# Kernel optimization log

Measured on AMD Instinct MI355X. Metric: run time of the kernel, lower is better.

The kernel has to match this reference:

```python
import jax, jax.numpy as jnp
import numpy as np

EPS = 1e-12  # F.normalize default eps


def _l2_normalize(x):
    # F.normalize(x, p=2) normalizes over dim=1 (channels) by default
    n = jnp.sqrt(jnp.sum(x * x, axis=1, keepdims=True))
    return x / jnp.maximum(n, EPS)


def _cost_volume(left, right, num_disp):
    # left, right: (N, C, H, W)
    l = _l2_normalize(left)
    r = _l2_normalize(right)
    # dot[n,h,x,y] = sum_c l[n,c,h,x] * r[n,c,h,y]   -> (N, H, W, W)
    dot = jnp.einsum('nchx,nchy->nhxy', l, r)
    W = left.shape[-1]
    x = jnp.arange(W)                                   # (W,)
    j = jnp.arange(num_disp)                            # (D,)
    # torch.diagonal(offset=-j) + F.pad((j,0)) picks dot[..., x, x-j] with zeros for x<j
    idx = jnp.clip(x[None, :] - j[:, None], 0, W - 1)   # (D, W)
    g = dot[:, :, x[None, :], idx]                      # (N, H, D, W)
    valid = (x[None, :] >= j[:, None])                  # (D, W)
    g = jnp.where(valid[None, None, :, :], g, jnp.zeros((), dtype=g.dtype))
    return jnp.transpose(g, (0, 2, 1, 3))               # (N, D, H, W)


def setup_inputs() -> dict:
    key = jax.random.key(0)
    ks = jax.random.split(key, 6)
    shapes = [(2, 32, 256, 512), (2, 64, 128, 256), (2, 96, 64, 128)]
    inp = {}
    for i, s in enumerate(shapes):
        inp[f'left{i}'] = jax.random.normal(ks[2 * i], s, dtype=jnp.float32)
        inp[f'right{i}'] = jax.random.normal(ks[2 * i + 1], s, dtype=jnp.float32)
    inp['max_disparity'] = 128
    return inp


def reference(left0, right0, left1, right1, left2, right2, max_disparity):
    lefts = [left0, left1, left2]
    rights = [right0, right1, right2]
    md = min(int(max_disparity), lefts[0].shape[-1])
    cost_volumes = []
    for i, (l, r) in enumerate(zip(lefts, rights)):
        cost_volumes.append(_cost_volume(l, r, md // (2 ** i)))
    return tuple(cost_volumes)
```

## Files before the change

kernel.cpp:

```cpp
#include <hip/hip_runtime.h>

typedef __attribute__((ext_vector_type(8))) short bf16x8;
typedef __attribute__((ext_vector_type(4))) float f32x4;

static __device__ __forceinline__ unsigned short f32_to_bf16(float f) {
    unsigned int x = __float_as_uint(f);
    x += 0x7fffu + ((x >> 16) & 1u);
    return (unsigned short)(x >> 16);
}

template<int C, int H, int W, int D, int TX, int NT>
__global__ __launch_bounds__(NT)
void cost_volume_mfma(const float* __restrict__ Lp, const float* __restrict__ Rp,
                      float* __restrict__ out)
{
    constexpr int RS = TX + D;
    constexpr int AS = C + 8;
    constexpr int KC = C / 32;
    constexpr int NW = NT / 64;
    static_assert(NW == TX / 16, "one wave per 16-wide x-tile");
    static_assert((AS * 2) % 16 == 0, "frag rows must be 16B aligned");

    constexpr int STAGE_F = C * (TX + RS);
    constexpr int OBUF_F  = D * TX;
    constexpr int UNION_F = STAGE_F > OBUF_F ? STAGE_F : OBUF_F;

    __shared__ __align__(16) float uni[UNION_F];
    __shared__ __align__(16) unsigned short Abf[RS * AS];
    __shared__ __align__(16) unsigned short Bbf[TX * AS];

    float* lsf  = uni;
    float* rsf  = uni + C * TX;
    float* obuf = uni;

    const int tid = threadIdx.x;
    constexpr int NXB = W / TX;
    const int bx = blockIdx.x;
    const int xb = bx % NXB;
    const int h  = (bx / NXB) % H;
    const int n  = bx / (NXB * H);
    const int X0 = xb * TX;

    for (int i = tid; i < C * TX / 4; i += NT) {
        const int c = i / (TX / 4), v = i % (TX / 4);
        *(float4*)&lsf[c * TX + 4 * v] =
            *(const float4*)&Lp[(((size_t)n * C + c) * H + h) * W + X0 + 4 * v];
    }
    for (int i = tid; i < C * RS / 4; i += NT) {
        const int c = i / (RS / 4), v = i % (RS / 4);
        const int y = X0 - D + 4 * v;
        const float* src = &Rp[(((size_t)n * C + c) * H + h) * W];
        float4 val;
        if (y >= 0) val = *(const float4*)&src[y];
        else {
            val.x = (y + 0) >= 0 ? src[y + 0] : 0.f;
            val.y = (y + 1) >= 0 ? src[y + 1] : 0.f;
            val.z = (y + 2) >= 0 ? src[y + 2] : 0.f;
            val.w = (y + 3) >= 0 ? src[y + 3] : 0.f;
        }
        *(float4*)&rsf[c * RS + 4 * v] = val;
    }
    __syncthreads();

    for (int col = tid; col < TX + RS; col += NT) {
        const float* src; int stride; unsigned short* dst;
        if (col < TX) { src = lsf + col;        stride = TX; dst = Bbf + col * AS; }
        else          { src = rsf + (col - TX); stride = RS; dst = Abf + (col - TX) * AS; }
        float v[C];
        float s = 0.f;
        #pragma unroll
        for (int c = 0; c < C; ++c) { v[c] = src[c * stride]; s += v[c] * v[c]; }
        const float inv = 1.0f / fmaxf(sqrtf(s), 1e-12f);
        #pragma unroll
        for (int c0 = 0; c0 < C; c0 += 8) {
            union { unsigned short us[8]; uint4 q; } p;
            #pragma unroll
            for (int k = 0; k < 8; ++k) p.us[k] = f32_to_bf16(v[c0 + k] * inv);
            *(uint4*)&dst[c0] = p.q;
        }
    }
    __syncthreads();

    const int wave = tid >> 6, lane = tid & 63;
    const int colc = lane & 15, quad = lane >> 4;

    bf16x8 bfr[KC];
    #pragma unroll
    for (int kc = 0; kc < KC; ++kc)
        bfr[kc] = *(const bf16x8*)&Bbf[(wave * 16 + colc) * AS + kc * 32 + quad * 8];

    const int xl = wave * 16 + colc;
    #pragma unroll
    for (int t = 0; t <= D / 16; ++t) {
        const int yt = wave + t;
        f32x4 acc = {0.f, 0.f, 0.f, 0.f};
        #pragma unroll
        for (int kc = 0; kc < KC; ++kc) {
            const bf16x8 a =
                *(const bf16x8*)&Abf[(yt * 16 + colc) * AS + kc * 32 + quad * 8];
            acc = __builtin_amdgcn_mfma_f32_16x16x32_bf16(a, bfr[kc], acc, 0, 0, 0);
        }
        const int jb = D + xl - yt * 16 - quad * 4;
        #pragma unroll
        for (int r = 0; r < 4; ++r) {
            const int j = jb - r;
            if (j >= 0 && j < D) obuf[j * TX + xl] = acc[r];
        }
    }
    __syncthreads();

    constexpr int JV = TX / 4;
    for (int i = tid; i < D * TX / 4; i += NT) {
        const int j = i / JV, c4 = i % JV;
        *(float4*)&out[(((size_t)n * D + j) * H + h) * W + X0 + 4 * c4] =
            *(const float4*)&obuf[j * TX + 4 * c4];
    }
}

extern "C" void kernel_launch(void* const* d_in, const int* in_sizes, int n_in,
                              void* d_out, int out_size, void* d_ws, size_t ws_size,
                              hipStream_t stream) {
    (void)in_sizes; (void)n_in; (void)d_ws; (void)ws_size; (void)out_size;
    const float* l0 = (const float*)d_in[0];
    const float* r0 = (const float*)d_in[1];
    const float* l1 = (const float*)d_in[2];
    const float* r1 = (const float*)d_in[3];
    const float* l2 = (const float*)d_in[4];
    const float* r2 = (const float*)d_in[5];

    float* o0 = (float*)d_out;
    float* o1 = o0 + (size_t)2 * 128 * 256 * 512;
    float* o2 = o1 + (size_t)2 * 64 * 128 * 256;

    cost_volume_mfma<32, 256, 512, 128, 64, 256>
        <<<2 * 256 * (512 / 64), 256, 0, stream>>>(l0, r0, o0);
    cost_volume_mfma<64, 128, 256, 64, 32, 128>
        <<<2 * 128 * (256 / 32), 128, 0, stream>>>(l1, r1, o1);
    cost_volume_mfma<96, 64, 128, 32, 32, 128>
        <<<2 * 64 * (128 / 32), 128, 0, stream>>>(l2, r2, o2);
}
```

Before: 313.9 us.

## Fuse three cost-volume launches into one kernel with direct bf16 staging

Merges the three per-scale kernels into a single launch and remaps blocks with an XCD-aware swizzle. Each thread now loads one column straight from global memory into bf16 LDS, which removes the fp32 staging buffer and one sync. L2 normalisation is applied after the MFMA as per-row and per-column scale factors. The output tile is staged in LDS as swizzled fp16, which halves LDS traffic but adds fp16 rounding to the outputs. Scales 1 and 2 now use TX=64 with 256 threads.

```diff
diff --git a/kernel.cpp b/kernel.cpp
--- a/kernel.cpp
+++ b/kernel.cpp
@@ -2,6 +2,7 @@
 
 typedef __attribute__((ext_vector_type(8))) short bf16x8;
 typedef __attribute__((ext_vector_type(4))) float f32x4;
+typedef __attribute__((ext_vector_type(4))) _Float16 f16x4;
 
 static __device__ __forceinline__ unsigned short f32_to_bf16(float f) {
     unsigned int x = __float_as_uint(f);
@@ -9,75 +10,63 @@
     return (unsigned short)(x >> 16);
 }
 
+static constexpr int SMEM_BYTES = 38400;
+
 template<int C, int H, int W, int D, int TX, int NT>
-__global__ __launch_bounds__(NT)
-void cost_volume_mfma(const float* __restrict__ Lp, const float* __restrict__ Rp,
-                      float* __restrict__ out)
+__device__ __forceinline__
+void cv_body(const int bx, const float* __restrict__ Lp, const float* __restrict__ Rp,
+             float* __restrict__ out, char* smem)
 {
     constexpr int RS = TX + D;
     constexpr int AS = C + 8;
     constexpr int KC = C / 32;
     constexpr int NW = NT / 64;
-    static_assert(NW == TX / 16, "one wave per 16-wide x-tile");
-    static_assert((AS * 2) % 16 == 0, "frag rows must be 16B aligned");
+    static_assert(NW == TX / 16, "one wave per 16-wide x-strip");
+    static_assert(TX + RS <= NT, "staging: one column per thread");
+    static_assert(TX == 64, "obuf swizzle assumes 128B rows; wave-aligned branch split");
+    static_assert(RS * AS * 2 + TX * AS * 2 + (RS + TX) * 4 + D * TX * 2 <= SMEM_BYTES, "lds");
 
-    constexpr int STAGE_F = C * (TX + RS);
-    constexpr int OBUF_F  = D * TX;
-    constexpr int UNION_F = STAGE_F > OBUF_F ? STAGE_F : OBUF_F;
-
-    __shared__ __align__(16) float uni[UNION_F];
-    __shared__ __align__(16) unsigned short Abf[RS * AS];
-    __shared__ __align__(16) unsigned short Bbf[TX * AS];
-
-    float* lsf  = uni;
-    float* rsf  = uni + C * TX;
-    float* obuf = uni;
+    unsigned short* Abf = (unsigned short*)smem;
+    unsigned short* Bbf = Abf + RS * AS;
+    float* invA = (float*)(Bbf + TX * AS);
+    float* invB = invA + RS;
+    char*  obuf = (char*)(invB + TX);
 
     const int tid = threadIdx.x;
     constexpr int NXB = W / TX;
-    const int bx = blockIdx.x;
     const int xb = bx % NXB;
     const int h  = (bx / NXB) % H;
     const int n  = bx / (NXB * H);
     const int X0 = xb * TX;
 
-    for (int i = tid; i < C * TX / 4; i += NT) {
-        const int c = i / (TX / 4), v = i % (TX / 4);
-        *(float4*)&lsf[c * TX + 4 * v] =
-            *(const float4*)&Lp[(((size_t)n * C + c) * H + h) * W + X0 + 4 * v];
-    }
-    for (int i = tid; i < C * RS / 4; i += NT) {
-        const int c = i / (RS / 4), v = i % (RS / 4);
-        const int y = X0 - D + 4 * v;
-        const float* src = &Rp[(((size_t)n * C + c) * H + h) * W];
-        float4 val;
-        if (y >= 0) val = *(const float4*)&src[y];
-        else {
-            val.x = (y + 0) >= 0 ? src[y + 0] : 0.f;
-            val.y = (y + 1) >= 0 ? src[y + 1] : 0.f;
-            val.z = (y + 2) >= 0 ? src[y + 2] : 0.f;
-            val.w = (y + 3) >= 0 ? src[y + 3] : 0.f;
+    const size_t CH = (size_t)H * W;
+    const float* Lb = Lp + ((size_t)n * C * H + h) * W;
+    const float* Rb = Rp + ((size_t)n * C * H + h) * W;
+
+    const int col = tid;
+    if (col < TX + RS) {
+        const float* src; unsigned short* dst; int g; bool zero;
+        if (col < TX) { g = X0 + col;            src = Lb; dst = Bbf + col * AS;        zero = false; }
+        else          { g = X0 - D + (col - TX); src = Rb; dst = Abf + (col - TX) * AS; zero = g < 0; }
+        float ssq = 0.f;
+        if (!zero) {
+            #pragma unroll
+            for (int c0 = 0; c0 < C; c0 += 8) {
+                float v[8];
+                #pragma unroll
+                for (int k = 0; k < 8; ++k) v[k] = src[(size_t)(c0 + k) * CH + g];
+                union { unsigned short us[8]; uint4 q; } p;
+                #pragma unroll
+                for (int k = 0; k < 8; ++k) { ssq += v[k] * v[k]; p.us[k] = f32_to_bf16(v[k]); }
+                *(uint4*)&dst[c0] = p.q;
+            }
+        } else {
+            const uint4 z = {0u, 0u, 0u, 0u};
+            #pragma unroll
+            for (int c0 = 0; c0 < C; c0 += 8) *(uint4*)&dst[c0] = z;
         }
-        *(float4*)&rsf[c * RS + 4 * v] = val;
-    }
-    __syncthreads();
-
-    for (int col = tid; col < TX + RS; col += NT) {
-        const float* src; int stride; unsigned short* dst;
-        if (col < TX) { src = lsf + col;        stride = TX; dst = Bbf + col * AS; }
-        else          { src = rsf + (col - TX); stride = RS; dst = Abf + (col - TX) * AS; }
-        float v[C];
-        float s = 0.f;
-        #pragma unroll
-        for (int c = 0; c < C; ++c) { v[c] = src[c * stride]; s += v[c] * v[c]; }
-        const float inv = 1.0f / fmaxf(sqrtf(s), 1e-12f);
-        #pragma unroll
-        for (int c0 = 0; c0 < C; c0 += 8) {
-            union { unsigned short us[8]; uint4 q; } p;
-            #pragma unroll
-            for (int k = 0; k < 8; ++k) p.us[k] = f32_to_bf16(v[c0 + k] * inv);
-            *(uint4*)&dst[c0] = p.q;
-        }
+        const float inv = 1.0f / fmaxf(sqrtf(ssq), 1e-12f);
+        if (col < TX) invB[col] = inv; else invA[col - TX] = inv;
     }
     __syncthreads();
 
@@ -90,31 +79,64 @@
         bfr[kc] = *(const bf16x8*)&Bbf[(wave * 16 + colc) * AS + kc * 32 + quad * 8];
 
     const int xl = wave * 16 + colc;
+    const float sB = invB[xl];
+
     #pragma unroll
     for (int t = 0; t <= D / 16; ++t) {
         const int yt = wave + t;
         f32x4 acc = {0.f, 0.f, 0.f, 0.f};
         #pragma unroll
         for (int kc = 0; kc < KC; ++kc) {
-            const bf16x8 a =
-                *(const bf16x8*)&Abf[(yt * 16 + colc) * AS + kc * 32 + quad * 8];
+            const bf16x8 a = *(const bf16x8*)&Abf[(yt * 16 + colc) * AS + kc * 32 + quad * 8];
             acc = __builtin_amdgcn_mfma_f32_16x16x32_bf16(a, bfr[kc], acc, 0, 0, 0);
         }
-        const int jb = D + xl - yt * 16 - quad * 4;
+        const int yb = yt * 16 + quad * 4;
+        const int jb = D + xl - yb;
         #pragma unroll
         for (int r = 0; r < 4; ++r) {
             const int j = jb - r;
-            if (j >= 0 && j < D) obuf[j * TX + xl] = acc[r];
+            if (j >= 0 && j < D) {
+                const float val = acc[r] * sB * invA[yb + r];
+                *(_Float16*)(obuf + (((j * TX + xl) * 2) ^ ((j & 7) << 4))) = (_Float16)val;
+            }
         }
     }
     __syncthreads();
 
-    constexpr int JV = TX / 4;
-    for (int i = tid; i < D * TX / 4; i += NT) {
-        const int j = i / JV, c4 = i % JV;
-        *(float4*)&out[(((size_t)n * D + j) * H + h) * W + X0 + 4 * c4] =
-            *(const float4*)&obuf[j * TX + 4 * c4];
+    constexpr int NIT = D * TX / 4 / NT;
+    float* orow = out + ((size_t)n * D) * CH + (size_t)h * W + X0;
+    #pragma unroll
+    for (int it = 0; it < NIT; ++it) {
+        const int idx = it * NT + tid;
+        const int j = idx >> 4, xo = idx & 15;
+        const f16x4 hv = *(const f16x4*)(obuf + (((j * TX + xo * 4) * 2) ^ ((j & 7) << 4)));
+        float4 o;
+        o.x = (float)hv.x; o.y = (float)hv.y; o.z = (float)hv.z; o.w = (float)hv.w;
+        *(float4*)&orow[(size_t)j * CH + xo * 4] = o;
     }
+}
+
+constexpr int G0 = 2 * 256 * (512 / 64);
+constexpr int G1 = 2 * 128 * (256 / 64);
+constexpr int G2 = 2 * 64  * (128 / 64);
+
+static __device__ __forceinline__ int xcd_swz(int b, int nwg) {
+    return (b & 7) * (nwg >> 3) + (b >> 3);
+}
+
+__global__ __launch_bounds__(256, 4)
+void fused_cv(const float* __restrict__ l0, const float* __restrict__ r0, float* __restrict__ o0,
+              const float* __restrict__ l1, const float* __restrict__ r1, float* __restrict__ o1,
+              const float* __restrict__ l2, const float* __restrict__ r2, float* __restrict__ o2)
+{
+    __shared__ __align__(16) char smem[SMEM_BYTES];
+    const int bid = blockIdx.x;
+    if (bid < G0)
+        cv_body<32, 256, 512, 128, 64, 256>(xcd_swz(bid, G0), l0, r0, o0, smem);
+    else if (bid < G0 + G1)
+        cv_body<64, 128, 256,  64, 64, 256>(xcd_swz(bid - G0, G1), l1, r1, o1, smem);
+    else
+        cv_body<96,  64, 128,  32, 64, 256>(xcd_swz(bid - G0 - G1, G2), l2, r2, o2, smem);
 }
 
 extern "C" void kernel_launch(void* const* d_in, const int* in_sizes, int n_in,
@@ -132,10 +154,5 @@
     float* o1 = o0 + (size_t)2 * 128 * 256 * 512;
     float* o2 = o1 + (size_t)2 * 64 * 128 * 256;
 
-    cost_volume_mfma<32, 256, 512, 128, 64, 256>
-        <<<2 * 256 * (512 / 64), 256, 0, stream>>>(l0, r0, o0);
-    cost_volume_mfma<64, 128, 256, 64, 32, 128>
-        <<<2 * 128 * (256 / 32), 128, 0, stream>>>(l1, r1, o1);
-    cost_volume_mfma<96, 64, 128, 32, 32, 128>
-        <<<2 * 64 * (128 / 32), 128, 0, stream>>>(l2, r2, o2);
+    fused_cv<<<G0 + G1 + G2, 256, 0, stream>>>(l0, r0, o0, l1, r1, o1, l2, r2, o2);
 }
```

Result: faster. 254.8 us (-18.8%).
